# Kernel optimization log

Hardware: AMD Instinct MI355X
Metric: run time of the kernel (lower is better)

The kernel has to match this reference:

```python
import jax, jax.numpy as jnp
import numpy as np

# Model hyperparameters (from init_kwargs)
D_MODEL, D_STATE, D_CONV, EXPAND, NHEADS, NGROUPS = 1024, 16, 4, 2, 8, 1
D_INNER = D_MODEL * EXPAND                      # 2048
HEADDIM = D_INNER // NHEADS                     # 256
D_XBC = D_INNER + 2 * NGROUPS * D_STATE         # conv channels: x + B + C
D_IN_PROJ = 3 * D_INNER + D_XBC + NHEADS        # z0 + x0 + z(unused) + xBC + dt
BATCH, SEQLEN = 2, 2048
LN_EPS = 1e-5


def setup_inputs() -> dict:
    key = jax.random.key(0)
    ks = jax.random.split(key, 8)
    u = jax.random.normal(ks[0], (BATCH, SEQLEN, D_MODEL), dtype=jnp.float32)
    W_in = jax.random.normal(ks[1], (D_IN_PROJ, D_MODEL), jnp.float32) / np.sqrt(D_MODEL)
    conv_w = jax.random.normal(ks[2], (D_XBC, 1, D_CONV), jnp.float32) / np.sqrt(D_CONV)
    conv_b = jnp.zeros((D_XBC,), jnp.float32)
    # dt_bias = inverse-softplus of dt ~ LogUniform(1e-3, 1e-1), as in source init
    dt = jnp.exp(jax.random.uniform(ks[3], (NHEADS,)) * (np.log(0.1) - np.log(0.001)) + np.log(0.001))
    dt_bias = dt + jnp.log(-jnp.expm1(-dt))
    A_log = jnp.log(jax.random.uniform(ks[4], (NHEADS,), minval=0.9, maxval=0.999))
    D_param = jnp.ones((NHEADS,), jnp.float32)
    ln_gamma = jnp.ones((D_INNER,), jnp.float32)
    ln_beta = jnp.zeros((D_INNER,), jnp.float32)
    W_gate = jax.random.normal(ks[5], (D_INNER, D_INNER), jnp.float32) / np.sqrt(D_INNER)
    b_gate = jnp.zeros((D_INNER,), jnp.float32)
    W_out = jax.random.normal(ks[6], (D_MODEL, 2 * D_INNER), jnp.float32) / np.sqrt(2 * D_INNER)
    return dict(u=u, W_in=W_in, conv_w=conv_w, conv_b=conv_b, dt_bias=dt_bias,
                A_log=A_log, D_param=D_param, ln_gamma=ln_gamma, ln_beta=ln_beta,
                W_gate=W_gate, b_gate=b_gate, W_out=W_out)


def _silu(x):
    return x * jax.nn.sigmoid(x)


def reference(u, W_in, conv_w, conv_b, dt_bias, A_log, D_param,
              ln_gamma, ln_beta, W_gate, b_gate, W_out):
    B, L, _ = u.shape
    zxbcdt = u @ W_in.T                                   # [B,L,D_IN_PROJ]
    z0 = zxbcdt[..., :D_INNER]
    x0 = zxbcdt[..., D_INNER:2 * D_INNER]
    # z = zxbcdt[..., 2*D_INNER:3*D_INNER]  # split but never used in source forward
    xBC = zxbcdt[..., 3 * D_INNER:3 * D_INNER + D_XBC]
    dt = jax.nn.softplus(zxbcdt[..., -NHEADS:] + dt_bias)  # [B,L,H]
    A = -jnp.exp(A_log)                                    # [H], per-head scalar

    # causal depthwise conv1d over time (left pad d_conv-1, crop to L)
    xBC_c = jnp.transpose(xBC, (0, 2, 1))                  # [B,C,L]
    xBC_c = jax.lax.conv_general_dilated(
        xBC_c, conv_w, window_strides=(1,), padding=[(D_CONV - 1, 0)],
        dimension_numbers=('NCH', 'OIH', 'NCH'), feature_group_count=D_XBC)
    xBC = _silu(jnp.transpose(xBC_c, (0, 2, 1)) + conv_b)  # [B,L,C]

    x = xBC[..., :D_INNER].reshape(B, L, NHEADS, HEADDIM)  # [B,L,H,P]
    Bm = xBC[..., D_INNER:D_INNER + D_STATE]               # [B,L,N] (ngroups=1)
    Cm = xBC[..., D_INNER + D_STATE:]                      # [B,L,N]

    def step(h, inp):
        x_t, B_t, C_t, dt_t = inp                          # [B,H,P],[B,N],[B,N],[B,H]
        dA = jnp.exp(dt_t * A)[:, :, None, None]           # [B,H,1,1]
        h = dA * h + (dt_t[:, :, None, None] * x_t[..., None]) * B_t[:, None, None, :]
        y_t = jnp.einsum('bhpn,bn->bhp', h, C_t) + D_param[None, :, None] * x_t
        return h, y_t

    h0 = jnp.zeros((B, NHEADS, HEADDIM, D_STATE), u.dtype)
    xs = (jnp.moveaxis(x, 1, 0), jnp.moveaxis(Bm, 1, 0),
          jnp.moveaxis(Cm, 1, 0), jnp.moveaxis(dt, 1, 0))
    _, y = jax.lax.scan(step, h0, xs)                      # [L,B,H,P]
    y = jnp.moveaxis(y, 0, 1).reshape(B, L, D_INNER)

    # LayerNorm
    mu = y.mean(-1, keepdims=True)
    var = ((y - mu) ** 2).mean(-1, keepdims=True)
    y = (y - mu) * jax.lax.rsqrt(var + LN_EPS) * ln_gamma + ln_beta

    gate = jax.nn.sigmoid(y @ W_gate.T + b_gate)
    y = gate * y

    mlp_skip = _silu(z0) * x0
    return jnp.concatenate([mlp_skip, y], axis=-1) @ W_out.T  # [B,L,D_MODEL]
```

## Files before the change

### kernel.cpp

```cpp
#include <hip/hip_runtime.h>
#include <hip/hip_bf16.h>
#include <math.h>

#define BATCH   2
#define SEQLEN  2048
#define DMODEL  1024
#define DINNER  2048
#define DSTATE  16
#define NHEADS  8
#define HEADDIM 256
#define DXBC    2080
#define NPACK   6184
#define NPAD    6400
#define MROWS   4096
#define CHUNK   64
#define NCHUNK  32
#define BH      16

typedef unsigned int u32;
typedef unsigned short u16;
typedef __attribute__((ext_vector_type(8))) short short8;
typedef __attribute__((ext_vector_type(4))) float f32x4;

#define GLOAD16(g, l) __builtin_amdgcn_global_load_lds( \
    (const __attribute__((address_space(1))) u32*)(g),  \
    (__attribute__((address_space(3))) u32*)(l), 16, 0, 0)

#define MFMA_B16(d, a, b) d = __builtin_amdgcn_mfma_f32_16x16x32_bf16(a, b, d, 0, 0, 0)

__device__ __forceinline__ u16 f2bf(float f) {
  union { float f; u32 u; } v; v.f = f;
  u32 r = v.u + 0x7fff + ((v.u >> 16) & 1);
  return (u16)(r >> 16);
}
__device__ __forceinline__ float bf2f(u16 b) {
  union { u32 u; float f; } v; v.u = ((u32)b) << 16;
  return v.f;
}

struct GParts { float* p0; float* p1; };

#define S_U   1048576
#define S_WG  1048576
#define S_WO  1048576
#define S_WP  1638400
#define S_TOT (S_U + S_WG + S_WO + S_WP)

__global__ void cvt_all(const float* __restrict__ u, const float* __restrict__ Wg,
                        const float* __restrict__ Wo, const float* __restrict__ Win,
                        u16* __restrict__ ub, u16* __restrict__ Wgb,
                        u16* __restrict__ Wob, u16* __restrict__ Wp) {
  for (int i = blockIdx.x * 256 + threadIdx.x; i < S_TOT; i += gridDim.x * 256) {
    const float* src; u16* dst; int idx;
    if (i < S_U) { src = u; dst = ub; idx = i; }
    else if (i < S_U + S_WG) { src = Wg; dst = Wgb; idx = i - S_U; }
    else if (i < S_U + S_WG + S_WO) { src = Wo; dst = Wob; idx = i - S_U - S_WG; }
    else {
      int j = i - S_U - S_WG - S_WO;
      int row = j >> 8, c4 = j & 255;
      ushort4 o = make_ushort4(0, 0, 0, 0);
      if (row < NPACK) {
        int orig = row < 4096 ? row : row + 2048;
        float4 v = ((const float4*)(Win + (size_t)orig * DMODEL))[c4];
        o = make_ushort4(f2bf(v.x), f2bf(v.y), f2bf(v.z), f2bf(v.w));
      }
      ((ushort4*)Wp)[j] = o;
      continue;
    }
    float4 v = ((const float4*)src)[idx];
    ((ushort4*)dst)[idx] = make_ushort4(f2bf(v.x), f2bf(v.y), f2bf(v.z), f2bf(v.w));
  }
}

template <int NL>
__device__ __forceinline__ void stage_rows(const u16* __restrict__ gsrc, int ldk,
                                           char* ldsmat, int row0, int w, int l) {
  const int rl = w * 8 + (l >> 3);
  const int q = ((l & 7) ^ (l >> 3)) * 8;
  #pragma unroll
  for (int j = 0; j < NL; ++j) {
    GLOAD16(gsrc + (size_t)(row0 + j * 64 + rl) * ldk + q,
            ldsmat + (row0 + j * 64 + w * 8) * 128);
  }
}

__device__ __forceinline__ short8 frag8(const char* mat, int row, int q) {
  return *(const short8*)(mat + row * 128 + ((q ^ (row & 7)) << 4));
}

__global__ __launch_bounds__(512, 1) void gemmA(
    const u16* __restrict__ A, const u16* __restrict__ B, int K, int ldk,
    int ldo, u16* __restrict__ outp) {
  __shared__ char lds[131072];
  const int tid = threadIdx.x;
  const int w = tid >> 6, l = tid & 63;
  const int wm = w >> 2, wn = w & 3;
  const int fr = l & 15, g = l >> 4;
  int s = blockIdx.y * gridDim.x + blockIdx.x;
  const int nwg = gridDim.x * gridDim.y;
  s = (s & 7) * (nwg >> 3) + (s >> 3);
  const int bx = s % gridDim.x, by = s / gridDim.x;
  const u16* Ap = A + (size_t)bx * 256 * ldk;
  const u16* Bp = B + (size_t)by * 256 * ldk;
  const int NT = K >> 6;

  f32x4 acc[8][4];
  #pragma unroll
  for (int m = 0; m < 8; ++m)
    #pragma unroll
    for (int n = 0; n < 4; ++n) acc[m][n] = (f32x4){0.f, 0.f, 0.f, 0.f};

  stage_rows<2>(Bp, ldk, lds + 32768, 0, w, l);
  stage_rows<2>(Bp, ldk, lds + 32768, 128, w, l);
  stage_rows<1>(Ap, ldk, lds, 0, w, l);
  stage_rows<1>(Ap, ldk, lds, 128, w, l);
  stage_rows<1>(Ap, ldk, lds, 64, w, l);
  stage_rows<1>(Ap, ldk, lds, 192, w, l);

  for (int t = 0; t < NT; ++t) {
    const bool last = (t == NT - 1);
    const char* cbA = lds + (t & 1) * 65536;
    const char* cbB = cbA + 32768;
    char* nbA = lds + ((t + 1) & 1) * 65536;
    char* nbB = nbA + 32768;
    const u16* An = Ap + (size_t)(t + 1) * 64;
    const u16* Bn = Bp + (size_t)(t + 1) * 64;

    asm volatile("s_waitcnt vmcnt(2)" ::: "memory");
    __builtin_amdgcn_s_barrier();
    __builtin_amdgcn_sched_barrier(0);

    short8 bf0[4], bf1[4];
    #pragma unroll
    for (int n = 0; n < 4; ++n) {
      bf0[n] = frag8(cbB, wn * 64 + n * 16 + fr, g);
      bf1[n] = frag8(cbB, wn * 64 + n * 16 + fr, 4 + g);
    }
    {
      short8 a00 = frag8(cbA, wm * 128 + fr, g);
      short8 a01 = frag8(cbA, wm * 128 + fr, 4 + g);
      short8 a10 = frag8(cbA, wm * 128 + 16 + fr, g);
      short8 a11 = frag8(cbA, wm * 128 + 16 + fr, 4 + g);
      if (!last) stage_rows<2>(Bn, ldk, nbB, 0, w, l);
      __builtin_amdgcn_sched_barrier(0);
      __builtin_amdgcn_s_setprio(1);
      #pragma unroll
      for (int n = 0; n < 4; ++n) { MFMA_B16(acc[0][n], a00, bf0[n]); MFMA_B16(acc[1][n], a10, bf0[n]); }
      #pragma unroll
      for (int n = 0; n < 4; ++n) { MFMA_B16(acc[0][n], a01, bf1[n]); MFMA_B16(acc[1][n], a11, bf1[n]); }
      __builtin_amdgcn_s_setprio(0);
    }
    {
      short8 a00 = frag8(cbA, wm * 128 + 32 + fr, g);
      short8 a01 = frag8(cbA, wm * 128 + 32 + fr, 4 + g);
      short8 a10 = frag8(cbA, wm * 128 + 48 + fr, g);
      short8 a11 = frag8(cbA, wm * 128 + 48 + fr, 4 + g);
      if (!last) stage_rows<2>(Bn, ldk, nbB, 128, w, l);
      __builtin_amdgcn_sched_barrier(0);
      __builtin_amdgcn_s_setprio(1);
      #pragma unroll
      for (int n = 0; n < 4; ++n) { MFMA_B16(acc[2][n], a00, bf0[n]); MFMA_B16(acc[3][n], a10, bf0[n]); }
      #pragma unroll
      for (int n = 0; n < 4; ++n) { MFMA_B16(acc[2][n], a01, bf1[n]); MFMA_B16(acc[3][n], a11, bf1[n]); }
      __builtin_amdgcn_s_setprio(0);
    }
    if (last) { asm volatile("s_waitcnt vmcnt(0)" ::: "memory"); }
    else      { asm volatile("s_waitcnt vmcnt(4)" ::: "memory"); }
    __builtin_amdgcn_s_barrier();
    __builtin_amdgcn_sched_barrier(0);
    {
      short8 a00 = frag8(cbA, wm * 128 + 64 + fr, g);
      short8 a01 = frag8(cbA, wm * 128 + 64 + fr, 4 + g);
      short8 a10 = frag8(cbA, wm * 128 + 80 + fr, g);
      short8 a11 = frag8(cbA, wm * 128 + 80 + fr, 4 + g);
      if (!last) { stage_rows<1>(An, ldk, nbA, 0, w, l); stage_rows<1>(An, ldk, nbA, 128, w, l); }
      __builtin_amdgcn_sched_barrier(0);
      __builtin_amdgcn_s_setprio(1);
      #pragma unroll
      for (int n = 0; n < 4; ++n) { MFMA_B16(acc[4][n], a00, bf0[n]); MFMA_B16(acc[5][n], a10, bf0[n]); }
      #pragma unroll
      for (int n = 0; n < 4; ++n) { MFMA_B16(acc[4][n], a01, bf1[n]); MFMA_B16(acc[5][n], a11, bf1[n]); }
      __builtin_amdgcn_s_setprio(0);
    }
    {
      short8 a00 = frag8(cbA, wm * 128 + 96 + fr, g);
      short8 a01 = frag8(cbA, wm * 128 + 96 + fr, 4 + g);
      short8 a10 = frag8(cbA, wm * 128 + 112 + fr, g);
      short8 a11 = frag8(cbA, wm * 128 + 112 + fr, 4 + g);
      if (!last) { stage_rows<1>(An, ldk, nbA, 64, w, l); stage_rows<1>(An, ldk, nbA, 192, w, l); }
      __builtin_amdgcn_sched_barrier(0);
      __builtin_amdgcn_s_setprio(1);
      #pragma unroll
      for (int n = 0; n < 4; ++n) { MFMA_B16(acc[6][n], a00, bf0[n]); MFMA_B16(acc[7][n], a10, bf0[n]); }
      #pragma unroll
      for (int n = 0; n < 4; ++n) { MFMA_B16(acc[6][n], a01, bf1[n]); MFMA_B16(acc[7][n], a11, bf1[n]); }
      __builtin_amdgcn_s_setprio(0);
    }
  }

  const int er = g * 4;
  #pragma unroll
  for (int m = 0; m < 8; ++m)
    #pragma unroll
    for (int n = 0; n < 4; ++n)
      #pragma unroll
      for (int j = 0; j < 4; ++j) {
        int row = bx * 256 + wm * 128 + m * 16 + er + j;
        int col = by * 256 + wn * 64 + n * 16 + fr;
        outp[(size_t)row * ldo + col] = f2bf(acc[m][n][j]);
      }
}

template <int EPI, int MAP>
__global__ __launch_bounds__(512, 1) void gemmB(
    const u16* __restrict__ A, const u16* __restrict__ B, int K_loop, int ldk,
    int ldo, void* __restrict__ outp, const float* __restrict__ bias,
    const u16* __restrict__ gate_in, GParts gp) {
  __shared__ char lds[3 * 49152];
  const int tid = threadIdx.x;
  const int w = tid >> 6, l = tid & 63;
  const int wm = w >> 1, wn = w & 1;
  const int fr = l & 15, g = l >> 4;
  int bx, by;
  if (MAP == 1) {
    int b = blockIdx.y * gridDim.x + blockIdx.x;
    int r = b >> 3;
    bx = 2 * (b & 7) + (r >> 4);
    by = r & 15;
  } else {
    int s = blockIdx.y * gridDim.x + blockIdx.x;
    const int nwg = gridDim.x * gridDim.y;
    s = (s & 7) * (nwg >> 3) + (s >> 3);
    bx = s % gridDim.x; by = s / gridDim.x;
  }
  const u16* Ap = A + (size_t)bx * 256 * ldk + (size_t)blockIdx.z * K_loop;
  const u16* Bp = B + (size_t)by * 128 * ldk + (size_t)blockIdx.z * K_loop;
  const int NT = K_loop >> 6;

  f32x4 acc[4][4];
  #pragma unroll
  for (int m = 0; m < 4; ++m)
    #pragma unroll
    for (int n = 0; n < 4; ++n) acc[m][n] = (f32x4){0.f, 0.f, 0.f, 0.f};

  #pragma unroll
  for (int p = 0; p < 2; ++p) {
    char* bA = lds + p * 49152;
    char* bB = bA + 32768;
    const u16* Ak = Ap + (size_t)p * 64;
    const u16* Bk = Bp + (size_t)p * 64;
    stage_rows<1>(Bk, ldk, bB, 0, w, l);
    stage_rows<1>(Bk, ldk, bB, 64, w, l);
    stage_rows<1>(Ak, ldk, bA, 0, w, l);
    stage_rows<1>(Ak, ldk, bA, 64, w, l);
    stage_rows<1>(Ak, ldk, bA, 128, w, l);
    stage_rows<1>(Ak, ldk, bA, 192, w, l);
  }

  int cur = 0;
  for (int t = 0; t < NT; ++t) {
    const bool last = (t == NT - 1);
    const bool dostage = (t + 2 < NT);
    int st = cur + 2; if (st >= 3) st -= 3;
    const char* cbA = lds + cur * 49152;
    const char* cbB = cbA + 32768;
    char* nbA = lds + st * 49152;
    char* nbB = nbA + 32768;
    const u16* An = Ap + (size_t)(t + 2) * 64;
    const u16* Bn = Bp + (size_t)(t + 2) * 64;

    if (last) { asm volatile("s_waitcnt vmcnt(0)" ::: "memory"); }
    else      { asm volatile("s_waitcnt vmcnt(6)" ::: "memory"); }
    __builtin_amdgcn_s_barrier();
    __builtin_amdgcn_sched_barrier(0);

    short8 bf0[4], bf1[4];
    #pragma unroll
    for (int n = 0; n < 4; ++n) {
      bf0[n] = frag8(cbB, wn * 64 + n * 16 + fr, g);
      bf1[n] = frag8(cbB, wn * 64 + n * 16 + fr, 4 + g);
    }
    {
      short8 a00 = frag8(cbA, wm * 64 + fr, g);
      short8 a01 = frag8(cbA, wm * 64 + fr, 4 + g);
      short8 a10 = frag8(cbA, wm * 64 + 16 + fr, g);
      short8 a11 = frag8(cbA, wm * 64 + 16 + fr, 4 + g);
      if (dostage) {
        stage_rows<1>(Bn, ldk, nbB, 0, w, l);
        stage_rows<1>(Bn, ldk, nbB, 64, w, l);
        stage_rows<1>(An, ldk, nbA, 0, w, l);
      }
      __builtin_amdgcn_sched_barrier(0);
      __builtin_amdgcn_s_setprio(1);
      #pragma unroll
      for (int n = 0; n < 4; ++n) { MFMA_B16(acc[0][n], a00, bf0[n]); MFMA_B16(acc[1][n], a10, bf0[n]); }
      #pragma unroll
      for (int n = 0; n < 4; ++n) { MFMA_B16(acc[0][n], a01, bf1[n]); MFMA_B16(acc[1][n], a11, bf1[n]); }
      __builtin_amdgcn_s_setprio(0);
    }
    {
      short8 a00 = frag8(cbA, wm * 64 + 32 + fr, g);
      short8 a01 = frag8(cbA, wm * 64 + 32 + fr, 4 + g);
      short8 a10 = frag8(cbA, wm * 64 + 48 + fr, g);
      short8 a11 = frag8(cbA, wm * 64 + 48 + fr, 4 + g);
      if (dostage) {
        stage_rows<1>(An, ldk, nbA, 64, w, l);
        stage_rows<1>(An, ldk, nbA, 128, w, l);
        stage_rows<1>(An, ldk, nbA, 192, w, l);
      }
      __builtin_amdgcn_sched_barrier(0);
      __builtin_amdgcn_s_setprio(1);
      #pragma unroll
      for (int n = 0; n < 4; ++n) { MFMA_B16(acc[2][n], a00, bf0[n]); MFMA_B16(acc[3][n], a10, bf0[n]); }
      #pragma unroll
      for (int n = 0; n < 4; ++n) { MFMA_B16(acc[2][n], a01, bf1[n]); MFMA_B16(acc[3][n], a11, bf1[n]); }
      __builtin_amdgcn_s_setprio(0);
    }
    cur = cur + 1; if (cur >= 3) cur = 0;
  }

  const int er = g * 4;
  float* pp = nullptr;
  if (EPI == 2) pp = blockIdx.z == 0 ? gp.p0 : gp.p1;
  #pragma unroll
  for (int m = 0; m < 4; ++m)
    #pragma unroll
    for (int n = 0; n < 4; ++n)
      #pragma unroll
      for (int j = 0; j < 4; ++j) {
        int row = bx * 256 + wm * 64 + m * 16 + er + j;
        int col = by * 128 + wn * 64 + n * 16 + fr;
        float v = acc[m][n][j];
        if (EPI == 1) {
          float gt = 1.f / (1.f + __expf(-(v + bias[col])));
          float nv = bf2f(gate_in[(size_t)row * 2048 + col]);
          ((u16*)outp)[(size_t)row * 4096 + 2048 + col] = f2bf(gt * nv);
        } else {
          pp[(size_t)row * ldo + col] = v;
        }
      }
}

__global__ void reduce2(const float* __restrict__ p0, const float* __restrict__ p1,
                        float* __restrict__ out) {
  const int n4 = MROWS * DMODEL / 4;
  for (int i = blockIdx.x * 256 + threadIdx.x; i < n4; i += gridDim.x * 256) {
    float4 a = ((const float4*)p0)[i];
    float4 b = ((const float4*)p1)[i];
    float4 o;
    o.x = a.x + b.x; o.y = a.y + b.y; o.z = a.z + b.z; o.w = a.w + b.w;
    ((float4*)out)[i] = o;
  }
}

#define NB_CONV 16640
#define NB_MLP  8192
#define NB_DT   128

__global__ void prep_kernel(const u16* __restrict__ zx, const float* __restrict__ cw,
                            const float* __restrict__ cb, u16* __restrict__ xc,
                            float* __restrict__ bc, u16* __restrict__ hcat,
                            const float* __restrict__ dt_bias, float* __restrict__ dtb) {
  int blk = blockIdx.x;
  if (blk < NB_CONV) {
    int idx = blk * 256 + threadIdx.x;
    int c2 = idx % (DXBC / 2);
    int m = idx / (DXBC / 2);
    int c = c2 * 2;
    int l = m & (SEQLEN - 1);
    const u16* col = zx + (size_t)m * NPAD + 4096 + c;
    float2 cbv = *(const float2*)(cb + c);
    float4 w0 = ((const float4*)cw)[c2 * 2];
    float4 w1 = ((const float4*)cw)[c2 * 2 + 1];
    float a0 = cbv.x, a1 = cbv.y;
    ushort2 t0 = *(const ushort2*)col;
    a0 += w0.w * bf2f(t0.x); a1 += w1.w * bf2f(t0.y);
    if (l >= 1) { ushort2 t = *(const ushort2*)(col - NPAD);     a0 += w0.z * bf2f(t.x); a1 += w1.z * bf2f(t.y); }
    if (l >= 2) { ushort2 t = *(const ushort2*)(col - 2 * NPAD); a0 += w0.y * bf2f(t.x); a1 += w1.y * bf2f(t.y); }
    if (l >= 3) { ushort2 t = *(const ushort2*)(col - 3 * NPAD); a0 += w0.x * bf2f(t.x); a1 += w1.x * bf2f(t.y); }
    float s0 = a0 / (1.f + __expf(-a0));
    float s1 = a1 / (1.f + __expf(-a1));
    if (c < DINNER) {
      ushort2 o; o.x = f2bf(s0); o.y = f2bf(s1);
      *(ushort2*)(xc + (size_t)m * DINNER + c) = o;
    } else {
      float2 o; o.x = s0; o.y = s1;
      *(float2*)(bc + (size_t)m * 32 + (c - DINNER)) = o;
    }
  } else if (blk < NB_CONV + NB_MLP) {
    int i = (blk - NB_CONV) * 256 + threadIdx.x;
    int m = i >> 9, c4 = (i & 511) * 4;
    const u16* row = zx + (size_t)m * NPAD;
    ushort4 zv = *(const ushort4*)(row + c4);
    ushort4 xv = *(const ushort4*)(row + 2048 + c4);
    float z0, x0;
    ushort4 o;
    z0 = bf2f(zv.x); x0 = bf2f(xv.x); o.x = f2bf(x0 * z0 / (1.f + __expf(-z0)));
    z0 = bf2f(zv.y); x0 = bf2f(xv.y); o.y = f2bf(x0 * z0 / (1.f + __expf(-z0)));
    z0 = bf2f(zv.z); x0 = bf2f(xv.z); o.z = f2bf(x0 * z0 / (1.f + __expf(-z0)));
    z0 = bf2f(zv.w); x0 = bf2f(xv.w); o.w = f2bf(x0 * z0 / (1.f + __expf(-z0)));
    *(ushort4*)(hcat + (size_t)m * 4096 + c4) = o;
  } else {
    int idx = (blk - NB_CONV - NB_MLP) * 256 + threadIdx.x;
    if (idx >= MROWS * NHEADS) return;
    int hd = idx & 7, m = idx >> 3;
    float raw = bf2f(zx[(size_t)m * NPAD + 6176 + hd]) + dt_bias[hd];
    float dtv = raw > 20.f ? raw : log1pf(expf(raw));
    dtb[idx] = dtv;
  }
}

__device__ __forceinline__ int xs_addr(int r, int p) {
  return r * 512 + ((((p >> 3) ^ ((r >> 3) & 3)) & 31) << 4) + (p & 7) * 2;
}
__device__ __forceinline__ int P_addr(int t, int s) {
  return t * 128 + ((((s >> 3) ^ (t & 7)) & 7) << 4) + (s & 7) * 2;
}

__device__ __forceinline__ void stage_x(u16* xs, const u16* __restrict__ xc,
                                        size_t base, int tid) {
  #pragma unroll
  for (int it = 0; it < 8; ++it) {
    int r = it * 8 + (tid >> 5);
    int pc = (tid & 31) * 8;
    short8 v = *(const short8*)(xc + base + (size_t)r * DINNER + pc);
    *(short8*)((char*)xs + xs_addr(r, pc)) = v;
  }
}

__device__ __forceinline__ short8 xfrag(const u16* xs, int k0, int g, int p) {
  short8 v;
  #pragma unroll
  for (int j = 0; j < 8; ++j) {
    int s = k0 + g * 8 + j;
    v[j] = *(const short*)((const char*)xs + xs_addr(s, p));
  }
  return v;
}

__global__ __launch_bounds__(256) void ssd_state(
    const u16* __restrict__ xc, const float* __restrict__ bcb,
    const float* __restrict__ dtb, const float* __restrict__ A_log,
    float* __restrict__ Sbuf, float* __restrict__ lcbuf) {
  __shared__ u16 xs[64 * 256];
  __shared__ float sLC[64], sDT[64];
  __shared__ float wBT[16][65];
  const int tid = threadIdx.x;
  const int bh = blockIdx.x >> 5, c = blockIdx.x & 31;
  const int b = bh >> 3, h = bh & 7;
  const size_t row0 = (size_t)b * SEQLEN + c * CHUNK;
  stage_x(xs, xc, row0 * DINNER + h * HEADDIM, tid);
  if (tid < 64) {
    float dtv = dtb[(row0 + tid) * NHEADS + h];
    float A = -__expf(A_log[h]);
    float s = dtv * A;
    #pragma unroll
    for (int off = 1; off < 64; off <<= 1) {
      float v = __shfl_up(s, off, 64);
      if (tid >= off) s += v;
    }
    sLC[tid] = s; sDT[tid] = dtv;
    lcbuf[(size_t)blockIdx.x * 64 + tid] = s;
  }
  __syncthreads();
  const float lc63 = sLC[63];
  for (int i = tid; i < 1024; i += 256) {
    int n = i & 15, t = i >> 4;
    float w = sDT[t] * __expf(lc63 - sLC[t]);
    wBT[n][t] = w * bcb[(row0 + t) * 32 + n];
  }
  __syncthreads();
  const int lane = tid & 63, w = tid >> 6;
  const int cl = lane & 15, g = lane >> 4;
  f32x4 acc[4];
  #pragma unroll
  for (int pt = 0; pt < 4; ++pt) acc[pt] = (f32x4){0.f, 0.f, 0.f, 0.f};
  #pragma unroll
  for (int kk = 0; kk < 2; ++kk) {
    int k0 = kk * 32;
    short8 af;
    #pragma unroll
    for (int j = 0; j < 8; ++j) af[j] = (short)f2bf(wBT[cl][k0 + g * 8 + j]);
    #pragma unroll
    for (int pt = 0; pt < 4; ++pt) {
      short8 bf = xfrag(xs, k0, g, (w * 4 + pt) * 16 + cl);
      acc[pt] = __builtin_amdgcn_mfma_f32_16x16x32_bf16(af, bf, acc[pt], 0, 0, 0);
    }
  }
  float* Sc = Sbuf + (size_t)blockIdx.x * 16 * 256;
  #pragma unroll
  for (int pt = 0; pt < 4; ++pt)
    #pragma unroll
    for (int j = 0; j < 4; ++j)
      Sc[(g * 4 + j) * 256 + (w * 4 + pt) * 16 + cl] = acc[pt][j];
}

__global__ __launch_bounds__(256) void ssd_combine(
    const float* __restrict__ Sbuf, const float* __restrict__ lcbuf,
    float* __restrict__ Sprev) {
  const int bh = blockIdx.x >> 4, seg = blockIdx.x & 15;
  const int idx = seg * 256 + threadIdx.x;
  float lam[NCHUNK], sv[NCHUNK];
  const size_t base = (size_t)bh * NCHUNK * 4096 + idx;
  #pragma unroll
  for (int c = 0; c < NCHUNK; ++c) {
    lam[c] = lcbuf[((size_t)bh * NCHUNK + c) * 64 + 63];
    sv[c] = Sbuf[base + (size_t)c * 4096];
  }
  #pragma unroll
  for (int c = 0; c < NCHUNK; ++c) lam[c] = __expf(lam[c]);
  float r = 0.f;
  #pragma unroll
  for (int c = 0; c < NCHUNK; ++c) {
    Sprev[base + (size_t)c * 4096] = r;
    r = lam[c] * r + sv[c];
  }
}

__global__ __launch_bounds__(256) void ssd_out(
    const u16* __restrict__ xc, const float* __restrict__ bcb,
    const float* __restrict__ dtb, const float* __restrict__ lcbuf,
    const float* __restrict__ Sprev, const float* __restrict__ D_par,
    u16* __restrict__ y) {
  __shared__ u16 xs[64 * 256];
  __shared__ u16 P[64 * 64];
  __shared__ u16 sB[64][17], sC[64][17], sCe[64][17];
  __shared__ u16 sSp[256][17];
  __shared__ float sLC[64], sDT[64];
  const int tid = threadIdx.x;
  const int bh = blockIdx.x >> 5, c = blockIdx.x & 31;
  const int b = bh >> 3, h = bh & 7;
  const size_t row0 = (size_t)b * SEQLEN + c * CHUNK;
  stage_x(xs, xc, row0 * DINNER + h * HEADDIM, tid);
  if (tid < 64) {
    sLC[tid] = lcbuf[(size_t)blockIdx.x * 64 + tid];
    sDT[tid] = dtb[(row0 + tid) * NHEADS + h];
  }
  for (int i = tid; i < 1024; i += 256) {
    int n = i & 15, t = i >> 4;
    float Bv = bcb[(row0 + t) * 32 + n];
    float Cv = bcb[(row0 + t) * 32 + 16 + n];
    float e = __expf(lcbuf[(size_t)blockIdx.x * 64 + t]);
    sB[t][n] = f2bf(Bv);
    sC[t][n] = f2bf(Cv);
    sCe[t][n] = f2bf(Cv * e);
  }
  {
    const float* Sp = Sprev + (size_t)blockIdx.x * 4096;
    int p = tid & 255;
    if (tid < 256) {
      #pragma unroll
      for (int n = 0; n < 16; ++n) sSp[p][n] = f2bf(Sp[n * 256 + p]);
    }
  }
  __syncthreads();

  const int lane = tid & 63, w = tid >> 6;
  const int cl = lane & 15, g = lane >> 4;

  f32x4 gacc[4];
  #pragma unroll
  for (int st = 0; st < 4; ++st) gacc[st] = (f32x4){0.f, 0.f, 0.f, 0.f};
  short8 afc = (short8){0, 0, 0, 0, 0, 0, 0, 0};
  if (g < 2) {
    #pragma unroll
    for (int j = 0; j < 8; ++j) afc[j] = (short)sC[w * 16 + cl][g * 8 + j];
  }
  #pragma unroll
  for (int st = 0; st < 4; ++st) {
    short8 bfb = (short8){0, 0, 0, 0, 0, 0, 0, 0};
    if (g < 2) {
      #pragma unroll
      for (int j = 0; j < 8; ++j) bfb[j] = (short)sB[st * 16 + cl][g * 8 + j];
    }
    gacc[st] = __builtin_amdgcn_mfma_f32_16x16x32_bf16(afc, bfb, gacc[st], 0, 0, 0);
  }
  #pragma unroll
  for (int st = 0; st < 4; ++st) {
    #pragma unroll
    for (int j = 0; j < 4; ++j) {
      int t = w * 16 + g * 4 + j;
      int s = st * 16 + cl;
      float v = 0.f;
      if (s <= t) v = gacc[st][j] * sDT[s] * __expf(sLC[t] - sLC[s]);
      *(u16*)((char*)P + P_addr(t, s)) = f2bf(v);
    }
  }
  asm volatile("s_waitcnt lgkmcnt(0)" ::: "memory");
  __builtin_amdgcn_sched_barrier(0);

  f32x4 acc[16];
  #pragma unroll
  for (int pt = 0; pt < 16; ++pt) acc[pt] = (f32x4){0.f, 0.f, 0.f, 0.f};
  #pragma unroll
  for (int kk = 0; kk < 2; ++kk) {
    int k0 = kk * 32;
    short8 ap = *(const short8*)((const char*)P + P_addr(w * 16 + cl, k0 + g * 8));
    #pragma unroll
    for (int pt = 0; pt < 16; ++pt) {
      short8 bf = xfrag(xs, k0, g, pt * 16 + cl);
      acc[pt] = __builtin_amdgcn_mfma_f32_16x16x32_bf16(ap, bf, acc[pt], 0, 0, 0);
    }
  }
  {
    short8 ae = (short8){0, 0, 0, 0, 0, 0, 0, 0};
    if (g < 2) {
      #pragma unroll
      for (int j = 0; j < 8; ++j) ae[j] = (short)sCe[w * 16 + cl][g * 8 + j];
    }
    #pragma unroll
    for (int pt = 0; pt < 16; ++pt) {
      short8 bs = (short8){0, 0, 0, 0, 0, 0, 0, 0};
      if (g < 2) {
        #pragma unroll
        for (int j = 0; j < 8; ++j) bs[j] = (short)sSp[pt * 16 + cl][g * 8 + j];
      }
      acc[pt] = __builtin_amdgcn_mfma_f32_16x16x32_bf16(ae, bs, acc[pt], 0, 0, 0);
    }
  }
  const float Dv = D_par[h];
  #pragma unroll
  for (int pt = 0; pt < 16; ++pt) {
    #pragma unroll
    for (int j = 0; j < 4; ++j) {
      int t = w * 16 + g * 4 + j;
      int p = pt * 16 + cl;
      float xv = bf2f(*(const u16*)((const char*)xs + xs_addr(t, p)));
      float v = acc[pt][j] + Dv * xv;
      y[(row0 + t) * DINNER + h * HEADDIM + p] = f2bf(v);
    }
  }
}

__global__ __launch_bounds__(256) void ln_kernel(const u16* __restrict__ y,
                                                 const float* __restrict__ gamma,
                                                 const float* __restrict__ beta,
                                                 u16* __restrict__ nrm) {
  const int row = blockIdx.x;
  const int t = threadIdx.x;
  const u16* yr = y + (size_t)row * DINNER;
  short8 v = *(const short8*)(yr + t * 8);
  float f[8];
  float s = 0.f, ss = 0.f;
  #pragma unroll
  for (int j = 0; j < 8; ++j) {
    f[j] = bf2f((u16)v[j]);
    s += f[j]; ss += f[j] * f[j];
  }
  #pragma unroll
  for (int o = 1; o < 64; o <<= 1) { s += __shfl_xor(s, o); ss += __shfl_xor(ss, o); }
  __shared__ float rs[4], rss[4];
  const int wid = t >> 6;
  if ((t & 63) == 0) { rs[wid] = s; rss[wid] = ss; }
  __syncthreads();
  s = rs[0] + rs[1] + rs[2] + rs[3];
  ss = rss[0] + rss[1] + rss[2] + rss[3];
  float mu = s * (1.f / DINNER);
  float var = ss * (1.f / DINNER) - mu * mu;
  float inv = rsqrtf(var + 1e-5f);
  float4 g0 = ((const float4*)gamma)[t * 2], g1 = ((const float4*)gamma)[t * 2 + 1];
  float4 b0 = ((const float4*)beta)[t * 2], b1 = ((const float4*)beta)[t * 2 + 1];
  short8 o;
  o[0] = (short)f2bf((f[0] - mu) * inv * g0.x + b0.x);
  o[1] = (short)f2bf((f[1] - mu) * inv * g0.y + b0.y);
  o[2] = (short)f2bf((f[2] - mu) * inv * g0.z + b0.z);
  o[3] = (short)f2bf((f[3] - mu) * inv * g0.w + b0.w);
  o[4] = (short)f2bf((f[4] - mu) * inv * g1.x + b1.x);
  o[5] = (short)f2bf((f[5] - mu) * inv * g1.y + b1.y);
  o[6] = (short)f2bf((f[6] - mu) * inv * g1.z + b1.z);
  o[7] = (short)f2bf((f[7] - mu) * inv * g1.w + b1.w);
  *(short8*)(nrm + (size_t)row * DINNER + t * 8) = o;
}

extern "C" void kernel_launch(void* const* d_in, const int* in_sizes, int n_in,
                              void* d_out, int out_size, void* d_ws, size_t ws_size,
                              hipStream_t stream) {
  (void)in_sizes; (void)n_in; (void)out_size; (void)ws_size;
  const float* u       = (const float*)d_in[0];
  const float* W_in    = (const float*)d_in[1];
  const float* conv_w  = (const float*)d_in[2];
  const float* conv_b  = (const float*)d_in[3];
  const float* dt_bias = (const float*)d_in[4];
  const float* A_log   = (const float*)d_in[5];
  const float* D_par   = (const float*)d_in[6];
  const float* ln_g    = (const float*)d_in[7];
  const float* ln_b    = (const float*)d_in[8];
  const float* W_gate  = (const float*)d_in[9];
  const float* b_gate  = (const float*)d_in[10];
  const float* W_out   = (const float*)d_in[11];
  float* out = (float*)d_out;

  size_t off = 0;
  auto take = [&](size_t bytes) -> char* {
    char* p = (char*)d_ws + off;
    off = (off + bytes + 255) & ~(size_t)255;
    return p;
  };
  u16* u16b  = (u16*)take((size_t)MROWS * DMODEL * 2);
  u16* Wp    = (u16*)take((size_t)NPAD * DMODEL * 2);
  u16* Wg    = (u16*)take((size_t)DINNER * DINNER * 2);
  u16* Wo    = (u16*)take((size_t)DMODEL * 2 * DINNER * 2);
  u16* zx    = (u16*)take((size_t)MROWS * NPAD * 2);
  u16* xc    = (u16*)take((size_t)MROWS * DINNER * 2);
  float* bcb = (float*)take((size_t)MROWS * 32 * 4);
  float* dtb = (float*)take((size_t)MROWS * NHEADS * 4);
  float* lcbuf = (float*)take((size_t)BH * NCHUNK * 64 * 4);
  u16* nrm   = (u16*)take((size_t)MROWS * DINNER * 2);
  u16* hcat  = (u16*)take((size_t)MROWS * 2 * DINNER * 2);

  float* Sbuf  = (float*)u16b;
  u16*   y     = zx;
  float* Sprev = (float*)((char*)zx + (size_t)16 * 1024 * 1024);
  GParts parts2;
  parts2.p0 = (float*)zx;
  parts2.p1 = (float*)((char*)zx + (size_t)16 * 1024 * 1024);
  GParts none = {nullptr, nullptr};

  cvt_all<<<4096, 256, 0, stream>>>(u, W_gate, W_out, W_in, u16b, Wg, Wo, Wp);

  gemmA<<<dim3(MROWS / 256, NPAD / 256), 512, 0, stream>>>(
      u16b, Wp, DMODEL, DMODEL, NPAD, zx);

  prep_kernel<<<NB_CONV + NB_MLP + NB_DT, 256, 0, stream>>>(
      zx, conv_w, conv_b, xc, bcb, hcat, dt_bias, dtb);

  ssd_state<<<BH * NCHUNK, 256, 0, stream>>>(xc, bcb, dtb, A_log, Sbuf, lcbuf);
  ssd_combine<<<BH * 16, 256, 0, stream>>>(Sbuf, lcbuf, Sprev);
  ssd_out<<<BH * NCHUNK, 256, 0, stream>>>(xc, bcb, dtb, lcbuf, Sprev, D_par, y);

  ln_kernel<<<MROWS, 256, 0, stream>>>(y, ln_g, ln_b, nrm);

  gemmB<1, 1><<<dim3(MROWS / 256, DINNER / 128), 512, 0, stream>>>(
      nrm, Wg, DINNER, DINNER, 0, hcat, b_gate, nrm, none);

  gemmB<2, 0><<<dim3(MROWS / 256, DMODEL / 128, 2), 512, 0, stream>>>(
      hcat, Wo, 2 * DINNER / 2, 2 * DINNER, DMODEL, nullptr, nullptr, nullptr, parts2);

  reduce2<<<2048, 256, 0, stream>>>(parts2.p0, parts2.p1, out);
}
```

Measured before the change: 242.1 us.

## Replace split-K output GEMM and reduction with single 128x128-tile GEMM

The final output projection used a split-K GEMM with 256x128 tiles writing two fp32 partial buffers, followed by a separate reduction kernel. It now uses a new full-K GEMM with 128x128 tiles, giving 32x8=256 workgroups, and writes fp32 results directly to the output. This removes the partial-buffer writes and reads and one kernel launch. In exchange, each workgroup runs twice as many K iterations, and the smaller tiles reuse each loaded operand less.

```diff
diff --git a/kernel.cpp b/kernel.cpp
--- a/kernel.cpp
+++ b/kernel.cpp
@@ -37,8 +37,6 @@
   union { u32 u; float f; } v; v.u = ((u32)b) << 16;
   return v.f;
 }
-
-struct GParts { float* p0; float* p1; };
 
 #define S_U   1048576
 #define S_WG  1048576
@@ -215,7 +213,7 @@
 __global__ __launch_bounds__(512, 1) void gemmB(
     const u16* __restrict__ A, const u16* __restrict__ B, int K_loop, int ldk,
     int ldo, void* __restrict__ outp, const float* __restrict__ bias,
-    const u16* __restrict__ gate_in, GParts gp) {
+    const u16* __restrict__ gate_in) {
   __shared__ char lds[3 * 49152];
   const int tid = threadIdx.x;
   const int w = tid >> 6, l = tid & 63;
@@ -233,8 +231,8 @@
     s = (s & 7) * (nwg >> 3) + (s >> 3);
     bx = s % gridDim.x; by = s / gridDim.x;
   }
-  const u16* Ap = A + (size_t)bx * 256 * ldk + (size_t)blockIdx.z * K_loop;
-  const u16* Bp = B + (size_t)by * 128 * ldk + (size_t)blockIdx.z * K_loop;
+  const u16* Ap = A + (size_t)bx * 256 * ldk;
+  const u16* Bp = B + (size_t)by * 128 * ldk;
   const int NT = K_loop >> 6;
 
   f32x4 acc[4][4];
@@ -320,8 +318,6 @@
   }
 
   const int er = g * 4;
-  float* pp = nullptr;
-  if (EPI == 2) pp = blockIdx.z == 0 ? gp.p0 : gp.p1;
   #pragma unroll
   for (int m = 0; m < 4; ++m)
     #pragma unroll
@@ -331,26 +327,92 @@
         int row = bx * 256 + wm * 64 + m * 16 + er + j;
         int col = by * 128 + wn * 64 + n * 16 + fr;
         float v = acc[m][n][j];
-        if (EPI == 1) {
-          float gt = 1.f / (1.f + __expf(-(v + bias[col])));
-          float nv = bf2f(gate_in[(size_t)row * 2048 + col]);
-          ((u16*)outp)[(size_t)row * 4096 + 2048 + col] = f2bf(gt * nv);
-        } else {
-          pp[(size_t)row * ldo + col] = v;
-        }
+        float gt = 1.f / (1.f + __expf(-(v + bias[col])));
+        float nv = bf2f(gate_in[(size_t)row * 2048 + col]);
+        ((u16*)outp)[(size_t)row * 4096 + 2048 + col] = f2bf(gt * nv);
       }
 }
 
-__global__ void reduce2(const float* __restrict__ p0, const float* __restrict__ p1,
-                        float* __restrict__ out) {
-  const int n4 = MROWS * DMODEL / 4;
-  for (int i = blockIdx.x * 256 + threadIdx.x; i < n4; i += gridDim.x * 256) {
-    float4 a = ((const float4*)p0)[i];
-    float4 b = ((const float4*)p1)[i];
-    float4 o;
-    o.x = a.x + b.x; o.y = a.y + b.y; o.z = a.z + b.z; o.w = a.w + b.w;
-    ((float4*)out)[i] = o;
-  }
+__global__ __launch_bounds__(512, 1) void gemmC(
+    const u16* __restrict__ A, const u16* __restrict__ B, int K, int ldk,
+    int ldo, float* __restrict__ outp) {
+  __shared__ char lds[3 * 32768];
+  const int tid = threadIdx.x;
+  const int w = tid >> 6, l = tid & 63;
+  const int wm = w >> 2, wn = w & 3;
+  const int fr = l & 15, g = l >> 4;
+  int s = blockIdx.y * gridDim.x + blockIdx.x;
+  const int nwg = gridDim.x * gridDim.y;
+  s = (s & 7) * (nwg >> 3) + (s >> 3);
+  const int bx = s % gridDim.x, by = s / gridDim.x;
+  const u16* Ap = A + (size_t)bx * 128 * ldk;
+  const u16* Bp = B + (size_t)by * 128 * ldk;
+  const int NT = K >> 6;
+
+  f32x4 acc[4][2];
+  #pragma unroll
+  for (int m = 0; m < 4; ++m)
+    #pragma unroll
+    for (int n = 0; n < 2; ++n) acc[m][n] = (f32x4){0.f, 0.f, 0.f, 0.f};
+
+  #pragma unroll
+  for (int p = 0; p < 2; ++p) {
+    char* nb = lds + p * 32768;
+    stage_rows<2>(Ap + (size_t)p * 64, ldk, nb, 0, w, l);
+    stage_rows<2>(Bp + (size_t)p * 64, ldk, nb + 16384, 0, w, l);
+  }
+
+  int cur = 0;
+  for (int t = 0; t < NT; ++t) {
+    const bool last = (t == NT - 1);
+    if (last) { asm volatile("s_waitcnt vmcnt(0)" ::: "memory"); }
+    else      { asm volatile("s_waitcnt vmcnt(4)" ::: "memory"); }
+    __builtin_amdgcn_s_barrier();
+    __builtin_amdgcn_sched_barrier(0);
+
+    const char* cbA = lds + cur * 32768;
+    const char* cbB = cbA + 16384;
+    short8 af[4][2], bfr[2][2];
+    #pragma unroll
+    for (int m = 0; m < 4; ++m) {
+      af[m][0] = frag8(cbA, wm * 64 + m * 16 + fr, g);
+      af[m][1] = frag8(cbA, wm * 64 + m * 16 + fr, 4 + g);
+    }
+    #pragma unroll
+    for (int n = 0; n < 2; ++n) {
+      bfr[n][0] = frag8(cbB, wn * 32 + n * 16 + fr, g);
+      bfr[n][1] = frag8(cbB, wn * 32 + n * 16 + fr, 4 + g);
+    }
+    if (t + 2 < NT) {
+      int st = cur + 2; if (st >= 3) st -= 3;
+      char* nb = lds + st * 32768;
+      stage_rows<2>(Ap + (size_t)(t + 2) * 64, ldk, nb, 0, w, l);
+      stage_rows<2>(Bp + (size_t)(t + 2) * 64, ldk, nb + 16384, 0, w, l);
+    }
+    __builtin_amdgcn_sched_barrier(0);
+    __builtin_amdgcn_s_setprio(1);
+    #pragma unroll
+    for (int m = 0; m < 4; ++m)
+      #pragma unroll
+      for (int n = 0; n < 2; ++n) {
+        MFMA_B16(acc[m][n], af[m][0], bfr[n][0]);
+        MFMA_B16(acc[m][n], af[m][1], bfr[n][1]);
+      }
+    __builtin_amdgcn_s_setprio(0);
+    cur = cur + 1; if (cur >= 3) cur = 0;
+  }
+
+  const int er = g * 4;
+  #pragma unroll
+  for (int m = 0; m < 4; ++m)
+    #pragma unroll
+    for (int n = 0; n < 2; ++n)
+      #pragma unroll
+      for (int j = 0; j < 4; ++j) {
+        int row = bx * 128 + wm * 64 + m * 16 + er + j;
+        int col = by * 128 + wn * 32 + n * 16 + fr;
+        outp[(size_t)row * ldo + col] = acc[m][n][j];
+      }
 }
 
 #define NB_CONV 16640
@@ -711,10 +773,6 @@
   float* Sbuf  = (float*)u16b;
   u16*   y     = zx;
   float* Sprev = (float*)((char*)zx + (size_t)16 * 1024 * 1024);
-  GParts parts2;
-  parts2.p0 = (float*)zx;
-  parts2.p1 = (float*)((char*)zx + (size_t)16 * 1024 * 1024);
-  GParts none = {nullptr, nullptr};
 
   cvt_all<<<4096, 256, 0, stream>>>(u, W_gate, W_out, W_in, u16b, Wg, Wo, Wp);
 
@@ -731,10 +789,8 @@
   ln_kernel<<<MROWS, 256, 0, stream>>>(y, ln_g, ln_b, nrm);
 
   gemmB<1, 1><<<dim3(MROWS / 256, DINNER / 128), 512, 0, stream>>>(
-      nrm, Wg, DINNER, DINNER, 0, hcat, b_gate, nrm, none);
-
-  gemmB<2, 0><<<dim3(MROWS / 256, DMODEL / 128, 2), 512, 0, stream>>>(
-      hcat, Wo, 2 * DINNER / 2, 2 * DINNER, DMODEL, nullptr, nullptr, nullptr, parts2);
-
-  reduce2<<<2048, 256, 0, stream>>>(parts2.p0, parts2.p1, out);
-}
+      nrm, Wg, DINNER, DINNER, 0, hcat, b_gate, nrm);
+
+  gemmC<<<dim3(MROWS / 128, DMODEL / 128), 512, 0, stream>>>(
+      hcat, Wo, 2 * DINNER, 2 * DINNER, DMODEL, out);
+}
```

Result: faster. 231.7 us (-4.3%).
